# Optimization experiments

Hardware: AMD Instinct MI355X
Metric: run time of the kernel (lower is better)

## Reference

```python
import jax, jax.numpy as jnp
from jax import lax
import numpy as np

B = 8192
HID = 128
FILT = 256  # stft filter length
HOP = 128
PAD = 64
NBINS = 129  # FILT//2 + 1


def setup_inputs() -> dict:
    key = jax.random.key(0)
    ks = jax.random.split(key, 16)
    def rn(k, shape, fan_in):
        return jax.random.normal(k, shape, dtype=jnp.float32) / np.sqrt(fan_in)
    inp = {
        "audio_input": jax.random.normal(ks[0], (B, 4160), dtype=jnp.float32),
        "hidden_state": jnp.zeros((B, HID), dtype=jnp.float32),
        "cell_state": jnp.zeros((B, HID), dtype=jnp.float32),
        # STFT forward basis: [2*NBINS, 1, FILT] (real then imag banks)
        "stft_w": rn(ks[1], (2 * NBINS, 1, FILT), FILT),
        # encoder: 4 conv1d layers (out, in, k), strides 1,2,2,1, pad 1
        "enc_w1": rn(ks[2], (128, 129, 3), 129 * 3), "enc_b1": jnp.zeros((128,), jnp.float32),
        "enc_w2": rn(ks[3], (64, 128, 3), 128 * 3), "enc_b2": jnp.zeros((64,), jnp.float32),
        "enc_w3": rn(ks[4], (64, 64, 3), 64 * 3),   "enc_b3": jnp.zeros((64,), jnp.float32),
        "enc_w4": rn(ks[5], (128, 64, 3), 64 * 3),  "enc_b4": jnp.zeros((128,), jnp.float32),
        # LSTMCell (PyTorch layout): gates order i,f,g,o
        "w_ih": rn(ks[6], (4 * HID, HID), HID), "w_hh": rn(ks[7], (4 * HID, HID), HID),
        "b_ih": jnp.zeros((4 * HID,), jnp.float32), "b_hh": jnp.zeros((4 * HID,), jnp.float32),
        # output head: Linear(128 -> 1) + sigmoid
        "out_w": rn(ks[8], (1, HID), HID), "out_b": jnp.zeros((1,), jnp.float32),
    }
    return inp


def _conv1d(x, w, b, stride, pad):
    # x: [N, C_in, L], w: [C_out, C_in, k]
    y = lax.conv_general_dilated(x, w, (stride,), [(pad, pad)],
                                 dimension_numbers=("NCH", "OIH", "NCH"))
    return y + b[None, :, None]


def reference(audio_input, hidden_state, cell_state, stft_w,
              enc_w1, enc_b1, enc_w2, enc_b2, enc_w3, enc_b3, enc_w4, enc_b4,
              w_ih, w_hh, b_ih, b_hh, out_w, out_b):
    b = audio_input.shape[0]
    # chunk i with context == audio_input[:, i*512 : i*512 + 576]
    chunks = jnp.stack([audio_input[:, i * 512:i * 512 + 576] for i in range(8)], axis=0)  # [8,B,576]
    x = chunks.reshape(8 * b, 576)
    # STFT: reflect pad 64 each side, conv stride 128 -> [8B, 258, 4]
    xp = jnp.pad(x, ((0, 0), (PAD, PAD)), mode="reflect")[:, None, :]
    spec = lax.conv_general_dilated(xp, stft_w, (HOP,), "VALID",
                                    dimension_numbers=("NCH", "OIH", "NCH"))
    mag = jnp.sqrt(spec[:, :NBINS] ** 2 + spec[:, NBINS:] ** 2)  # [8B,129,4]
    # encoder conv stack: 4 -> 4 -> 2 -> 1 -> 1 frames
    h1 = jax.nn.relu(_conv1d(mag, enc_w1, enc_b1, 1, 1))
    h2 = jax.nn.relu(_conv1d(h1, enc_w2, enc_b2, 2, 1))
    h3 = jax.nn.relu(_conv1d(h2, enc_w3, enc_b3, 2, 1))
    h4 = jax.nn.relu(_conv1d(h3, enc_w4, enc_b4, 1, 1))  # [8B,128,1]
    feats = h4[:, :, 0].reshape(8, b, HID)  # [8,B,128]

    def step(carry, x_t):
        h, c = carry
        gates = x_t @ w_ih.T + b_ih + h @ w_hh.T + b_hh  # [B,4H]
        i_g, f_g, g_g, o_g = jnp.split(gates, 4, axis=-1)
        c_new = jax.nn.sigmoid(f_g) * c + jax.nn.sigmoid(i_g) * jnp.tanh(g_g)
        h_new = jax.nn.sigmoid(o_g) * jnp.tanh(c_new)
        p = jax.nn.sigmoid(h_new @ out_w.T + out_b)  # [B,1]
        return (h_new, c_new), p

    (h_fin, c_fin), probs = lax.scan(step, (hidden_state, cell_state), feats)  # probs [8,B,1]
    # final = 1 - prod_i (1 - p_i), shape [B,1,1]
    final = (1.0 - jnp.prod(1.0 - probs, axis=0))[:, :, None]
    return final, h_fin, c_fin
```

## Files before the change

### kernel.cpp

```cpp
#include <hip/hip_runtime.h>
#include <hip/hip_bf16.h>
#include <math.h>

typedef __hip_bfloat16 bf16;
typedef __attribute__((ext_vector_type(4))) float f32x4;
typedef __attribute__((ext_vector_type(8))) short short8;
typedef __attribute__((ext_vector_type(4))) short short4v;

#define BATCH   8192
#define NTOT    65536
#define NW      262144
#define HID     128

__device__ __forceinline__ float b2f(bf16 v){ return __bfloat162float(v); }
__device__ __forceinline__ bf16  f2b(float v){ return __float2bfloat16(v); }
__device__ __forceinline__ short f2bs(float v){
  bf16 b = __float2bfloat16(v);
  return *reinterpret_cast<short*>(&b);
}
__device__ __forceinline__ float sigf(float x){ return 1.0f/(1.0f+__expf(-x)); }
__device__ __forceinline__ float tanhfast(float x){
  return 1.0f - 2.0f/(__expf(2.0f*x)+1.0f);
}

__global__ __launch_bounds__(256) void k_wcvt(
    const float* __restrict__ W, bf16* __restrict__ Wb)
{
  const int idx = blockIdx.x*256 + threadIdx.x;
  if (idx < 258*256) Wb[idx] = f2b(W[idx]);
}
__global__ __launch_bounds__(256) void k_w1cvt(
    const float* __restrict__ w1, bf16* __restrict__ w1b)
{
  const int idx = blockIdx.x*256 + threadIdx.x;
  if (idx >= 61440) return;
  const int dt = idx / 20480, rem = idx % 20480;
  const int cout = rem / 160, k = rem % 160;
  const float v = (k < 129) ? w1[(cout*129 + k)*3 + dt] : 0.f;
  w1b[idx] = f2b(v);
}
__global__ __launch_bounds__(256) void k_w2cvt(
    const float* __restrict__ w2, bf16* __restrict__ w2b)
{
  const int idx = blockIdx.x*256 + threadIdx.x;
  if (idx >= 24576) return;
  const int dt = idx >> 13, cout = (idx >> 7) & 63, k = idx & 127;
  w2b[idx] = f2b(w2[(cout*128 + k)*3 + dt]);
}
__global__ __launch_bounds__(256) void k_w34cvt(
    const float* __restrict__ w3, const float* __restrict__ w4,
    bf16* __restrict__ w3e, bf16* __restrict__ w4e)
{
  const int idx = blockIdx.x*256 + threadIdx.x;
  if (idx >= 16384) return;
  if (idx < 8192){
    const int row = idx >> 7, k = idx & 127;
    const int cin = k >> 1, t = k & 1;
    w3e[idx] = f2b(w3[(row*64 + cin)*3 + 1 + t]);
  } else {
    const int i2 = idx - 8192;
    const int row = i2 >> 6, cin = i2 & 63;
    w4e[i2] = f2b(w4[(row*64 + cin)*3 + 1]);
  }
}
__global__ __launch_bounds__(256) void k_wlcvt1(
    const float* __restrict__ whh, bf16* __restrict__ wl1)
{
  const int idx = blockIdx.x*256 + threadIdx.x;
  if (idx >= 65536) return;
  wl1[idx] = f2b(whh[idx]);
}
__global__ __launch_bounds__(256) void k_wlxcvt(
    const float* __restrict__ wih, bf16* __restrict__ wlx)
{
  const int idx = blockIdx.x*256 + threadIdx.x;
  if (idx >= 65536) return;
  wlx[idx] = f2b(wih[idx]);
}

__global__ __launch_bounds__(256) void k_stft3(
    const float* __restrict__ audio, const bf16* __restrict__ Wb,
    bf16* __restrict__ mag)
{
  __shared__ __align__(16) char ALDS[96*512];
  __shared__ __align__(16) bf16 refl[4*8*64];
  const int tid = threadIdx.x, lane = tid & 63, wq = tid >> 6;
  const int r0 = blockIdx.x * 4;
  const float* arow = audio + (size_t)(r0 + wq) * 4160;

  #pragma unroll
  for (int q = 0; q < 8; ++q){
    const int e = q*64 + lane;
    const int i = e >> 6, k = e & 63;
    refl[(wq*8 + i)*64 + k] = f2b(arow[512*i + 64 - k]);
  }

  const int kgo8 = (lane>>4)*8;
  short8 Bfrag[2][8];
  #pragma unroll
  for (int ng = 0; ng < 2; ++ng){
    const int wl = ng*16 + (lane & 15);
    const int i = wl >> 2, t = wl & 3;
    #pragma unroll
    for (int ks = 0; ks < 8; ++ks){
      const int kb = ks*32 + kgo8;
      if (t == 0 && kb < 64){
        Bfrag[ng][ks] = *(const short8*)(refl + (wq*8 + i)*64 + kb);
      } else {
        const float* src = arow + 512*i + 128*t - 64 + kb;
        const float4 v0 = *(const float4*)(src);
        const float4 v1 = *(const float4*)(src + 4);
        short8 s;
        s[0]=f2bs(v0.x); s[1]=f2bs(v0.y); s[2]=f2bs(v0.z); s[3]=f2bs(v0.w);
        s[4]=f2bs(v1.x); s[5]=f2bs(v1.y); s[6]=f2bs(v1.z); s[7]=f2bs(v1.w);
        Bfrag[ng][ks] = s;
      }
    }
  }

  const int kab = (lane>>4)*16;
  for (int pass = 0; pass < 3; ++pass){
    __syncthreads();
    for (int idx = tid; idx < 96*32; idx += 256){
      const int ar = idx >> 5;
      const int cb = (idx & 31) * 16;
      const int b3 = ar >> 5, reim = (ar >> 4) & 1, bl = ar & 15;
      int bin = pass*48 + b3*16 + bl;
      if (bin > 128) bin = 128;
      const int grow = bin + reim*129;
      int off = ar*512 + cb; off ^= ((ar&7)<<4);
      *(f32x4*)(ALDS + off) = *(const f32x4*)((const char*)Wb + grow*512 + cb);
    }
    __syncthreads();

    f32x4 accRe[3][2], accIm[3][2];
    #pragma unroll
    for (int b3 = 0; b3 < 3; ++b3)
      #pragma unroll
      for (int ng = 0; ng < 2; ++ng){
        accRe[b3][ng] = f32x4{0.f,0.f,0.f,0.f};
        accIm[b3][ng] = f32x4{0.f,0.f,0.f,0.f};
      }
    #pragma unroll
    for (int ks = 0; ks < 8; ++ks){
      #pragma unroll
      for (int b3 = 0; b3 < 3; ++b3){
        const int arRe = b3*32 + (lane & 15);
        const int arIm = arRe + 16;
        int offRe = arRe*512 + ks*64 + kab; offRe ^= ((arRe&7)<<4);
        int offIm = arIm*512 + ks*64 + kab; offIm ^= ((arIm&7)<<4);
        const short8 aRe = *(const short8*)(ALDS + offRe);
        const short8 aIm = *(const short8*)(ALDS + offIm);
        #pragma unroll
        for (int ng = 0; ng < 2; ++ng){
          accRe[b3][ng] = __builtin_amdgcn_mfma_f32_16x16x32_bf16(
              aRe, Bfrag[ng][ks], accRe[b3][ng], 0, 0, 0);
          accIm[b3][ng] = __builtin_amdgcn_mfma_f32_16x16x32_bf16(
              aIm, Bfrag[ng][ks], accIm[b3][ng], 0, 0, 0);
        }
      }
    }
    #pragma unroll
    for (int b3 = 0; b3 < 3; ++b3)
      #pragma unroll
      for (int j = 0; j < 4; ++j){
        const int bin = (pass*3 + b3)*16 + (lane>>4)*4 + j;
        if (bin <= 128){
          #pragma unroll
          for (int ng = 0; ng < 2; ++ng){
            const int wl = ng*16 + (lane & 15);
            const int i = wl >> 2, t = wl & 3;
            const float re = accRe[b3][ng][j], im = accIm[b3][ng][j];
            mag[(size_t)bin*NW + (size_t)i*32768 + (r0+wq)*4 + t] =
                f2b(sqrtf(re*re + im*im));
          }
        }
      }
  }
}

#define E1_LDS (192*320)
__global__ __launch_bounds__(256) void k_enc1234(
    const bf16* __restrict__ mag,
    const bf16* __restrict__ w1b, const float* __restrict__ b1,
    const bf16* __restrict__ w2b, const float* __restrict__ b2,
    const bf16* __restrict__ w3e, const float* __restrict__ b3,
    const bf16* __restrict__ w4e, const float* __restrict__ b4,
    bf16* __restrict__ h4)
{
  __shared__ __align__(16) char Bs[E1_LDS];
  char* const B3 = Bs + 40960;
  char* const B4 = Bs + 49152;
  const int tid = threadIdx.x, lane = tid & 63, wq = tid >> 6;
  const int n0 = blockIdx.x * 32;
  const int i  = n0 >> 13, b0 = n0 & 8191;
  const size_t colbase = (size_t)i*32768 + (size_t)b0*4;
  const int kb = (lane>>4)*16;
  const int wr = wq >> 1, wc = wq & 1;

  for (int off = tid*16; off < E1_LDS; off += 256*16)
    *(f32x4*)(Bs + off) = f32x4{0.f,0.f,0.f,0.f};
  __syncthreads();
  for (int it = tid; it < 129*64; it += 256){
    const int cin = it >> 6, seg = it & 63;
    const unsigned int pair =
        *(const unsigned int*)(mag + (size_t)cin*NW + colbase + seg*2);
    #pragma unroll
    for (int q = 0; q < 2; ++q){
      const int w = seg*2 + q;
      const int row = (w>>2)*6 + (w&3) + 1;
      int off = row*320 + cin*2; off ^= ((row&7)<<4);
      *(short*)(Bs + off) = (short)((q==0) ? (pair & 0xffff) : (pair >> 16));
    }
  }
  __syncthreads();

  f32x4 acc1[4][4];
  #pragma unroll
  for (int mg = 0; mg < 4; ++mg)
    #pragma unroll
    for (int ng = 0; ng < 4; ++ng) acc1[mg][ng] = f32x4{0.f,0.f,0.f,0.f};
  int brow[4], acol[4];
  #pragma unroll
  for (int ng = 0; ng < 4; ++ng){
    const int w = wc*64 + ng*16 + (lane & 15);
    brow[ng] = (w>>2)*6 + (w&3);
  }
  #pragma unroll
  for (int mg = 0; mg < 4; ++mg) acol[mg] = wr*64 + mg*16 + (lane & 15);

  for (int dt = 0; dt < 3; ++dt){
    #pragma unroll
    for (int ks = 0; ks < 5; ++ks){
      short8 afr[4], bfr[4];
      #pragma unroll
      for (int mg = 0; mg < 4; ++mg)
        afr[mg] = *(const short8*)((const char*)w1b +
            ((dt*128 + acol[mg])*160 + ks*32)*2 + kb);
      #pragma unroll
      for (int ng = 0; ng < 4; ++ng){
        const int row = brow[ng] + dt;
        int off = row*320 + ks*64 + kb; off ^= ((row&7)<<4);
        bfr[ng] = *(const short8*)(Bs + off);
      }
      #pragma unroll
      for (int mg = 0; mg < 4; ++mg)
        #pragma unroll
        for (int ng = 0; ng < 4; ++ng)
          acc1[mg][ng] = __builtin_amdgcn_mfma_f32_16x16x32_bf16(
              afr[mg], bfr[ng], acc1[mg][ng], 0, 0, 0);
    }
  }
  __syncthreads();

  for (int it = tid; it < 32*16; it += 256){
    const int nloc = it >> 4, cb = (it & 15)*16;
    *(f32x4*)(Bs + (nloc*5)*256 + cb) = f32x4{0.f,0.f,0.f,0.f};
  }
  #pragma unroll
  for (int mg = 0; mg < 4; ++mg)
    #pragma unroll
    for (int j = 0; j < 4; ++j){
      const int cout = wr*64 + mg*16 + (lane>>4)*4 + j;
      const float bv = b1[cout];
      #pragma unroll
      for (int ng = 0; ng < 4; ++ng){
        const int w = wc*64 + ng*16 + (lane & 15);
        float v = acc1[mg][ng][j] + bv; v = v > 0.f ? v : 0.f;
        const int row5 = (w>>2)*5 + (w&3) + 1;
        int off = row5*256 + cout*2; off ^= ((row5&7)<<4);
        *(short*)(Bs + off) = f2bs(v);
      }
    }
  __syncthreads();

  f32x4 acc2[2][2];
  #pragma unroll
  for (int mg = 0; mg < 2; ++mg)
    #pragma unroll
    for (int ng = 0; ng < 2; ++ng) acc2[mg][ng] = f32x4{0.f,0.f,0.f,0.f};
  int brow2[2], acol2[2];
  #pragma unroll
  for (int ng = 0; ng < 2; ++ng){
    const int wl = wc*32 + ng*16 + (lane & 15);
    brow2[ng] = (wl>>1)*5 + (wl&1)*2;
  }
  #pragma unroll
  for (int mg = 0; mg < 2; ++mg) acol2[mg] = wr*32 + mg*16 + (lane & 15);

  for (int dt = 0; dt < 3; ++dt){
    #pragma unroll
    for (int ks = 0; ks < 4; ++ks){
      short8 afr[2], bfr[2];
      #pragma unroll
      for (int mg = 0; mg < 2; ++mg)
        afr[mg] = *(const short8*)((const char*)w2b +
            ((dt*64 + acol2[mg])*128 + ks*32)*2 + kb);
      #pragma unroll
      for (int ng = 0; ng < 2; ++ng){
        const int row = brow2[ng] + dt;
        int off = row*256 + ks*64 + kb; off ^= ((row&7)<<4);
        bfr[ng] = *(const short8*)(Bs + off);
      }
      #pragma unroll
      for (int mg = 0; mg < 2; ++mg)
        #pragma unroll
        for (int ng = 0; ng < 2; ++ng)
          acc2[mg][ng] = __builtin_amdgcn_mfma_f32_16x16x32_bf16(
              afr[mg], bfr[ng], acc2[mg][ng], 0, 0, 0);
    }
  }

  #pragma unroll
  for (int mg = 0; mg < 2; ++mg)
    #pragma unroll
    for (int j = 0; j < 4; ++j){
      const int cout2 = wr*32 + mg*16 + (lane>>4)*4 + j;
      const float bv = b2[cout2];
      #pragma unroll
      for (int ng = 0; ng < 2; ++ng){
        const int wl = wc*32 + ng*16 + (lane & 15);
        float v = acc2[mg][ng][j] + bv; v = v > 0.f ? v : 0.f;
        const int nloc = wl >> 1, tp = wl & 1;
        int off = nloc*256 + (cout2*2 + tp)*2; off ^= ((nloc&7)<<4);
        *(short*)(B3 + off) = f2bs(v);
      }
    }
  __syncthreads();

  f32x4 acc3[2];
  acc3[0] = f32x4{0.f,0.f,0.f,0.f};
  acc3[1] = f32x4{0.f,0.f,0.f,0.f};
  const int ar1 = wq*16 + (lane & 15);
  #pragma unroll
  for (int ks = 0; ks < 4; ++ks){
    const short8 a = *(const short8*)((const char*)w3e + (ar1*128 + ks*32)*2 + kb);
    #pragma unroll
    for (int ng = 0; ng < 2; ++ng){
      const int row = ng*16 + (lane & 15);
      int off = row*256 + ks*64 + kb; off ^= ((row&7)<<4);
      const short8 bfr = *(const short8*)(B3 + off);
      acc3[ng] = __builtin_amdgcn_mfma_f32_16x16x32_bf16(a, bfr, acc3[ng], 0, 0, 0);
    }
  }

  #pragma unroll
  for (int j = 0; j < 4; ++j){
    const int r1 = wq*16 + (lane>>4)*4 + j;
    const float bv = b3[r1];
    #pragma unroll
    for (int ng = 0; ng < 2; ++ng){
      const int col = ng*16 + (lane & 15);
      float v = acc3[ng][j] + bv; v = v > 0.f ? v : 0.f;
      int off = col*128 + r1*2; off ^= ((col&7)<<4);
      *(short*)(B4 + off) = f2bs(v);
    }
  }
  __syncthreads();

  f32x4 acc4[2][2];
  #pragma unroll
  for (int mg = 0; mg < 2; ++mg)
    #pragma unroll
    for (int ng = 0; ng < 2; ++ng) acc4[mg][ng] = f32x4{0.f,0.f,0.f,0.f};
  #pragma unroll
  for (int ks = 0; ks < 2; ++ks){
    short8 bfr[2];
    #pragma unroll
    for (int ng = 0; ng < 2; ++ng){
      const int row = ng*16 + (lane & 15);
      int off = row*128 + ks*64 + kb; off ^= ((row&7)<<4);
      bfr[ng] = *(const short8*)(B4 + off);
    }
    #pragma unroll
    for (int mg = 0; mg < 2; ++mg){
      const int ar2 = wq*32 + mg*16 + (lane & 15);
      const short8 a = *(const short8*)((const char*)w4e + (ar2*64 + ks*32)*2 + kb);
      #pragma unroll
      for (int ng = 0; ng < 2; ++ng)
        acc4[mg][ng] = __builtin_amdgcn_mfma_f32_16x16x32_bf16(a, bfr[ng], acc4[mg][ng], 0, 0, 0);
    }
  }
  #pragma unroll
  for (int mg = 0; mg < 2; ++mg)
    #pragma unroll
    for (int j = 0; j < 4; ++j){
      const int cout = wq*32 + mg*16 + (lane>>4)*4 + j;
      const float bv = b4[cout];
      #pragma unroll
      for (int ng = 0; ng < 2; ++ng){
        const int n = n0 + ng*16 + (lane & 15);
        float v = acc4[mg][ng][j] + bv; v = v > 0.f ? v : 0.f;
        h4[(size_t)cout*NTOT + n] = f2b(v);
      }
    }
}

__global__ __launch_bounds__(256) void k_init(
    const float* __restrict__ h0, const float* __restrict__ c0,
    float* __restrict__ hT0, float* __restrict__ cT)
{
  const int idx = blockIdx.x*256 + threadIdx.x;
  const int b = idx >> 7, c = idx & 127;
  hT0[c*BATCH + b] = h0[idx];
  cT [c*BATCH + b] = c0[idx];
}

__global__ __launch_bounds__(256) void k_gatex(
    const bf16* __restrict__ h4, const bf16* __restrict__ wlx,
    float* __restrict__ xg, int half)
{
  __shared__ __align__(16) char Bs[32*256];
  const int tid = threadIdx.x, lane = tid & 63, wq = tid >> 6;
  const int n0 = blockIdx.x * 32;
  const int gcol = half*32768 + n0;

  for (int it = tid; it < 128*32; it += 256){
    const int cp = it >> 5, nl = it & 31;
    const bf16 v = h4[(size_t)cp*NTOT + gcol + nl];
    int off = nl*256 + cp*2; off ^= ((nl&7)<<4);
    *(short*)(Bs + off) = *(const short*)&v;
  }
  __syncthreads();

  f32x4 acc[8][2];
  #pragma unroll
  for (int mg = 0; mg < 8; ++mg)
    #pragma unroll
    for (int ng = 0; ng < 2; ++ng) acc[mg][ng] = f32x4{0.f,0.f,0.f,0.f};

  int arow[8];
  #pragma unroll
  for (int mg = 0; mg < 8; ++mg) arow[mg] = wq*128 + mg*16 + (lane & 15);
  const int kb = (lane>>4)*16;

  #pragma unroll
  for (int ks = 0; ks < 4; ++ks){
    short8 bfr[2];
    #pragma unroll
    for (int ng = 0; ng < 2; ++ng){
      const int row = ng*16 + (lane & 15);
      int off = row*256 + ks*64 + kb; off ^= ((row&7)<<4);
      bfr[ng] = *(const short8*)(Bs + off);
    }
    #pragma unroll
    for (int mg = 0; mg < 8; ++mg){
      const short8 a = *(const short8*)((const char*)wlx +
          ((size_t)arow[mg]*128 + ks*32)*2 + kb);
      #pragma unroll
      for (int ng = 0; ng < 2; ++ng)
        acc[mg][ng] = __builtin_amdgcn_mfma_f32_16x16x32_bf16(
            a, bfr[ng], acc[mg][ng], 0, 0, 0);
    }
  }

  #pragma unroll
  for (int mg = 0; mg < 8; ++mg)
    #pragma unroll
    for (int j = 0; j < 4; ++j){
      const int row = wq*128 + mg*16 + (lane>>4)*4 + j;
      #pragma unroll
      for (int ng = 0; ng < 2; ++ng){
        const int col = n0 + ng*16 + (lane & 15);
        xg[(size_t)row*32768 + col] = acc[mg][ng][j];
      }
    }
}

__global__ __launch_bounds__(256) void k_lstm_rec(
    const float* __restrict__ xg, const bf16* __restrict__ wl1,
    const float* __restrict__ bih, const float* __restrict__ bhh,
    const float* __restrict__ hprev, float* __restrict__ hout,
    float* __restrict__ cT, int s)
{
  __shared__ __align__(16) char Bs[32*256];
  const int tid = threadIdx.x, lane = tid & 63, wq = tid >> 6;
  const int b0 = blockIdx.x * 32;

  for (int it = tid; it < 128*32; it += 256){
    const int cp = it >> 5, bl = it & 31;
    const float v = hprev[cp*BATCH + b0 + bl];
    int off = bl*256 + cp*2; off ^= ((bl&7)<<4);
    *(short*)(Bs + off) = f2bs(v);
  }
  __syncthreads();

  const int c0r = wq*32;
  f32x4 acc[4][2][2];
  #pragma unroll
  for (int g = 0; g < 4; ++g)
    #pragma unroll
    for (int h = 0; h < 2; ++h)
      #pragma unroll
      for (int ng = 0; ng < 2; ++ng) acc[g][h][ng] = f32x4{0.f,0.f,0.f,0.f};

  int arow[4][2];
  #pragma unroll
  for (int g = 0; g < 4; ++g)
    #pragma unroll
    for (int h = 0; h < 2; ++h)
      arow[g][h] = (g*128 + c0r + h*16 + (lane&15))*256 + (lane>>4)*16;

  #pragma unroll
  for (int ks = 0; ks < 4; ++ks){
    short8 bfr[2];
    #pragma unroll
    for (int ng = 0; ng < 2; ++ng){
      const int row = ng*16 + (lane & 15);
      int off = row*256 + ks*64 + (lane>>4)*16; off ^= ((row&7)<<4);
      bfr[ng] = *(const short8*)(Bs + off);
    }
    #pragma unroll
    for (int g = 0; g < 4; ++g)
      #pragma unroll
      for (int h = 0; h < 2; ++h){
        const short8 a = *(const short8*)((const char*)wl1 + arow[g][h] + ks*64);
        #pragma unroll
        for (int ng = 0; ng < 2; ++ng)
          acc[g][h][ng] = __builtin_amdgcn_mfma_f32_16x16x32_bf16(
              a, bfr[ng], acc[g][h][ng], 0, 0, 0);
      }
  }

  const size_t xcolbase = (size_t)(s & 3)*8192 + b0;
  #pragma unroll
  for (int h = 0; h < 2; ++h)
    #pragma unroll
    for (int ng = 0; ng < 2; ++ng)
      #pragma unroll
      for (int j = 0; j < 4; ++j){
        const int c = c0r + h*16 + (lane>>4)*4 + j;
        const int b = b0 + ng*16 + (lane & 15);
        const size_t xc = xcolbase + ng*16 + (lane & 15);
        const float ig = acc[0][h][ng][j] + xg[(size_t)(0*128+c)*32768 + xc] + bih[c]       + bhh[c];
        const float fg = acc[1][h][ng][j] + xg[(size_t)(1*128+c)*32768 + xc] + bih[128 + c] + bhh[128 + c];
        const float gg = acc[2][h][ng][j] + xg[(size_t)(2*128+c)*32768 + xc] + bih[256 + c] + bhh[256 + c];
        const float og = acc[3][h][ng][j] + xg[(size_t)(3*128+c)*32768 + xc] + bih[384 + c] + bhh[384 + c];
        const float cold = cT[c*BATCH + b];
        const float cn = sigf(fg)*cold + sigf(ig)*tanhfast(gg);
        const float hn = sigf(og)*tanhfast(cn);
        cT  [c*BATCH + b] = cn;
        hout[c*BATCH + b] = hn;
      }
}

__global__ __launch_bounds__(256) void k_headp(
    const float* __restrict__ hseq, const float* __restrict__ ow,
    const float* __restrict__ ob, float* __restrict__ P)
{
  const int idx = blockIdx.x*256 + threadIdx.x;
  const int s = idx >> 13, b = idx & (BATCH-1);
  const float* hp = hseq + (size_t)s*HID*BATCH;
  float acc = ob[0];
  for (int c = 0; c < 128; ++c) acc += ow[c]*hp[c*BATCH + b];
  P[s*BATCH + b] = sigf(acc);
}
__global__ __launch_bounds__(256) void k_head2(
    const float* __restrict__ P, float* __restrict__ outp)
{
  const int b = blockIdx.x*256 + threadIdx.x;
  float prod = 1.f;
  #pragma unroll
  for (int s = 0; s < 8; ++s) prod *= (1.f - P[s*BATCH + b]);
  outp[b] = 1.f - prod;
}

__global__ __launch_bounds__(256) void k_outT(
    const float* __restrict__ h7, const float* __restrict__ cT,
    float* __restrict__ out)
{
  const int idx = blockIdx.x*256 + threadIdx.x;
  const int b = idx >> 7, c = idx & 127;
  out[8192 + idx]           = h7[c*BATCH + b];
  out[8192 + 1048576 + idx] = cT[c*BATCH + b];
}

extern "C" void kernel_launch(void* const* d_in, const int* in_sizes, int n_in,
                              void* d_out, int out_size, void* d_ws, size_t ws_size,
                              hipStream_t stream)
{
  (void)in_sizes; (void)n_in; (void)out_size; (void)ws_size;
  const float* audio = (const float*)d_in[0];
  const float* h0    = (const float*)d_in[1];
  const float* c0    = (const float*)d_in[2];
  const float* stftw = (const float*)d_in[3];
  const float* w1 = (const float*)d_in[4];  const float* b1 = (const float*)d_in[5];
  const float* w2 = (const float*)d_in[6];  const float* b2 = (const float*)d_in[7];
  const float* w3 = (const float*)d_in[8];  const float* b3 = (const float*)d_in[9];
  const float* w4 = (const float*)d_in[10]; const float* b4 = (const float*)d_in[11];
  const float* wih = (const float*)d_in[12]; const float* whh = (const float*)d_in[13];
  const float* bih = (const float*)d_in[14]; const float* bhh = (const float*)d_in[15];
  const float* ow  = (const float*)d_in[16]; const float* ob  = (const float*)d_in[17];
  float* out = (float*)d_out;

  char* ws = (char*)d_ws;
  bf16*  Wbf  = (bf16*) (ws + 67633152);
  bf16*  h4   = (bf16*) (ws + 67633152);
  bf16*  mag  = (bf16*) (ws + 0);
  float* xg   = (float*)(ws + 0);
  float* hseq = (float*)(ws + 92274688);
  float* hT0  = (float*)(ws + 125829120);
  float* cT   = (float*)(ws + 130023424);
  bf16*  w1b  = (bf16*) (ws + 134742016);
  bf16*  w2b  = (bf16*) (ws + 134864896);
  bf16*  w3e  = (bf16*) (ws + 134914048);
  bf16*  w4e  = (bf16*) (ws + 134930432);
  bf16*  wl1  = (bf16*) (ws + 134946816);
  bf16*  wlx  = (bf16*) (ws + 135077888);
  float* Pbuf = (float*)(ws + 135397376);

  k_wcvt  <<<258, 256, 0, stream>>>(stftw, Wbf);
  k_w1cvt <<<240, 256, 0, stream>>>(w1, w1b);
  k_w2cvt <<<96, 256, 0, stream>>>(w2, w2b);
  k_w34cvt<<<64, 256, 0, stream>>>(w3, w4, w3e, w4e);
  k_wlcvt1<<<256, 256, 0, stream>>>(whh, wl1);
  k_wlxcvt<<<256, 256, 0, stream>>>(wih, wlx);
  k_init  <<<4096, 256, 0, stream>>>(h0, c0, hT0, cT);
  k_stft3<<<2048, 256, 0, stream>>>(audio, Wbf, mag);
  k_enc1234<<<2048, 256, 0, stream>>>(mag, w1b, b1, w2b, b2, w3e, b3,
                                      w4e, b4, h4);
  for (int half = 0; half < 2; ++half){
    k_gatex<<<1024, 256, 0, stream>>>(h4, wlx, xg, half);
    for (int q = 0; q < 4; ++q){
      const int s = half*4 + q;
      const float* hprev = (s == 0) ? hT0 : (hseq + (size_t)(s-1)*HID*BATCH);
      k_lstm_rec<<<256, 256, 0, stream>>>(xg, wl1, bih, bhh, hprev,
                                          hseq + (size_t)s*HID*BATCH, cT, s);
    }
  }
  k_headp<<<256, 256, 0, stream>>>(hseq, ow, ob, Pbuf);
  k_head2<<<32, 256, 0, stream>>>(Pbuf, out);
  k_outT<<<4096, 256, 0, stream>>>(hseq + (size_t)7*HID*BATCH, cT, out);
}
```

Measured before the change: 435.4 us.

## Fuse all LSTM timesteps, head and output transpose into one persistent kernel

Replaces the eight per-step recurrent launches, the init transpose, the head kernels and the output transpose with one kernel. Each block keeps its 32-sample slice of h in LDS and c in registers across all eight steps, and accumulates the output-head probability product on chip. The input-gate buffer is enlarged to hold all eight steps so both gatex launches run before the recurrence. This removes repeated global round trips of h and c and about a dozen launches. In exchange, only 256 blocks do the whole sequential recurrence, a larger workspace is needed, and the final h and c are written with strided stores.

Result: no change. 430.0 us (-1.2%).

```diff
diff --git a/kernel.cpp b/kernel.cpp
--- a/kernel.cpp
+++ b/kernel.cpp
@@ -396,16 +396,6 @@
     }
 }
 
-__global__ __launch_bounds__(256) void k_init(
-    const float* __restrict__ h0, const float* __restrict__ c0,
-    float* __restrict__ hT0, float* __restrict__ cT)
-{
-  const int idx = blockIdx.x*256 + threadIdx.x;
-  const int b = idx >> 7, c = idx & 127;
-  hT0[c*BATCH + b] = h0[idx];
-  cT [c*BATCH + b] = c0[idx];
-}
-
 __global__ __launch_bounds__(256) void k_gatex(
     const bf16* __restrict__ h4, const bf16* __restrict__ wlx,
     float* __restrict__ xg, int half)
@@ -461,38 +451,48 @@
       const int row = wq*128 + mg*16 + (lane>>4)*4 + j;
       #pragma unroll
       for (int ng = 0; ng < 2; ++ng){
-        const int col = n0 + ng*16 + (lane & 15);
-        xg[(size_t)row*32768 + col] = acc[mg][ng][j];
-      }
-    }
-}
-
-__global__ __launch_bounds__(256) void k_lstm_rec(
+        const int col = gcol + ng*16 + (lane & 15);
+        xg[(size_t)row*65536 + col] = acc[mg][ng][j];
+      }
+    }
+}
+
+__global__ __launch_bounds__(256) void k_lstm_all2(
     const float* __restrict__ xg, const bf16* __restrict__ wl1,
     const float* __restrict__ bih, const float* __restrict__ bhh,
-    const float* __restrict__ hprev, float* __restrict__ hout,
-    float* __restrict__ cT, int s)
+    const float* __restrict__ h0, const float* __restrict__ c0,
+    const float* __restrict__ ow, const float* __restrict__ ob,
+    float* __restrict__ out)
 {
   __shared__ __align__(16) char Bs[32*256];
+  __shared__ float Ppart[16*32];
+  __shared__ float Pprod[32];
   const int tid = threadIdx.x, lane = tid & 63, wq = tid >> 6;
   const int b0 = blockIdx.x * 32;
+  const int c0r = wq*32;
 
   for (int it = tid; it < 128*32; it += 256){
     const int cp = it >> 5, bl = it & 31;
-    const float v = hprev[cp*BATCH + b0 + bl];
+    const float v = h0[(size_t)(b0 + bl)*128 + cp];
     int off = bl*256 + cp*2; off ^= ((bl&7)<<4);
     *(short*)(Bs + off) = f2bs(v);
   }
-  __syncthreads();
-
-  const int c0r = wq*32;
-  f32x4 acc[4][2][2];
-  #pragma unroll
-  for (int g = 0; g < 4; ++g)
-    #pragma unroll
-    for (int h = 0; h < 2; ++h)
-      #pragma unroll
-      for (int ng = 0; ng < 2; ++ng) acc[g][h][ng] = f32x4{0.f,0.f,0.f,0.f};
+  float cst[2][2][4], bsum[4][2][4], owv[2][4];
+  #pragma unroll
+  for (int h = 0; h < 2; ++h)
+    #pragma unroll
+    for (int j = 0; j < 4; ++j){
+      const int c = c0r + h*16 + (lane>>4)*4 + j;
+      owv[h][j] = ow[c];
+      #pragma unroll
+      for (int g = 0; g < 4; ++g)
+        bsum[g][h][j] = bih[g*128 + c] + bhh[g*128 + c];
+      #pragma unroll
+      for (int ng = 0; ng < 2; ++ng)
+        cst[h][ng][j] = c0[(size_t)(b0 + ng*16 + (lane & 15))*128 + c];
+    }
+  if (tid < 32) Pprod[tid] = 1.f;
+  const float obv = ob[0];
 
   int arow[4][2];
   #pragma unroll
@@ -501,78 +501,76 @@
     for (int h = 0; h < 2; ++h)
       arow[g][h] = (g*128 + c0r + h*16 + (lane&15))*256 + (lane>>4)*16;
 
-  #pragma unroll
-  for (int ks = 0; ks < 4; ++ks){
-    short8 bfr[2];
-    #pragma unroll
-    for (int ng = 0; ng < 2; ++ng){
-      const int row = ng*16 + (lane & 15);
-      int off = row*256 + ks*64 + (lane>>4)*16; off ^= ((row&7)<<4);
-      bfr[ng] = *(const short8*)(Bs + off);
-    }
+  __syncthreads();
+
+  for (int s = 0; s < 8; ++s){
+    f32x4 acc[4][2][2];
     #pragma unroll
     for (int g = 0; g < 4; ++g)
       #pragma unroll
-      for (int h = 0; h < 2; ++h){
-        const short8 a = *(const short8*)((const char*)wl1 + arow[g][h] + ks*64);
+      for (int h = 0; h < 2; ++h)
         #pragma unroll
-        for (int ng = 0; ng < 2; ++ng)
-          acc[g][h][ng] = __builtin_amdgcn_mfma_f32_16x16x32_bf16(
-              a, bfr[ng], acc[g][h][ng], 0, 0, 0);
-      }
-  }
-
-  const size_t xcolbase = (size_t)(s & 3)*8192 + b0;
-  #pragma unroll
-  for (int h = 0; h < 2; ++h)
-    #pragma unroll
-    for (int ng = 0; ng < 2; ++ng)
-      #pragma unroll
-      for (int j = 0; j < 4; ++j){
-        const int c = c0r + h*16 + (lane>>4)*4 + j;
-        const int b = b0 + ng*16 + (lane & 15);
-        const size_t xc = xcolbase + ng*16 + (lane & 15);
-        const float ig = acc[0][h][ng][j] + xg[(size_t)(0*128+c)*32768 + xc] + bih[c]       + bhh[c];
-        const float fg = acc[1][h][ng][j] + xg[(size_t)(1*128+c)*32768 + xc] + bih[128 + c] + bhh[128 + c];
-        const float gg = acc[2][h][ng][j] + xg[(size_t)(2*128+c)*32768 + xc] + bih[256 + c] + bhh[256 + c];
-        const float og = acc[3][h][ng][j] + xg[(size_t)(3*128+c)*32768 + xc] + bih[384 + c] + bhh[384 + c];
-        const float cold = cT[c*BATCH + b];
-        const float cn = sigf(fg)*cold + sigf(ig)*tanhfast(gg);
-        const float hn = sigf(og)*tanhfast(cn);
-        cT  [c*BATCH + b] = cn;
-        hout[c*BATCH + b] = hn;
-      }
-}
-
-__global__ __launch_bounds__(256) void k_headp(
-    const float* __restrict__ hseq, const float* __restrict__ ow,
-    const float* __restrict__ ob, float* __restrict__ P)
-{
-  const int idx = blockIdx.x*256 + threadIdx.x;
-  const int s = idx >> 13, b = idx & (BATCH-1);
-  const float* hp = hseq + (size_t)s*HID*BATCH;
-  float acc = ob[0];
-  for (int c = 0; c < 128; ++c) acc += ow[c]*hp[c*BATCH + b];
-  P[s*BATCH + b] = sigf(acc);
-}
-__global__ __launch_bounds__(256) void k_head2(
-    const float* __restrict__ P, float* __restrict__ outp)
-{
-  const int b = blockIdx.x*256 + threadIdx.x;
-  float prod = 1.f;
-  #pragma unroll
-  for (int s = 0; s < 8; ++s) prod *= (1.f - P[s*BATCH + b]);
-  outp[b] = 1.f - prod;
-}
-
-__global__ __launch_bounds__(256) void k_outT(
-    const float* __restrict__ h7, const float* __restrict__ cT,
-    float* __restrict__ out)
-{
-  const int idx = blockIdx.x*256 + threadIdx.x;
-  const int b = idx >> 7, c = idx & 127;
-  out[8192 + idx]           = h7[c*BATCH + b];
-  out[8192 + 1048576 + idx] = cT[c*BATCH + b];
+        for (int ng = 0; ng < 2; ++ng) acc[g][h][ng] = f32x4{0.f,0.f,0.f,0.f};
+    #pragma unroll
+    for (int ks = 0; ks < 4; ++ks){
+      short8 bfr[2];
+      #pragma unroll
+      for (int ng = 0; ng < 2; ++ng){
+        const int row = ng*16 + (lane & 15);
+        int off = row*256 + ks*64 + (lane>>4)*16; off ^= ((row&7)<<4);
+        bfr[ng] = *(const short8*)(Bs + off);
+      }
+      #pragma unroll
+      for (int g = 0; g < 4; ++g)
+        #pragma unroll
+        for (int h = 0; h < 2; ++h){
+          const short8 a = *(const short8*)((const char*)wl1 + arow[g][h] + ks*64);
+          #pragma unroll
+          for (int ng = 0; ng < 2; ++ng)
+            acc[g][h][ng] = __builtin_amdgcn_mfma_f32_16x16x32_bf16(
+                a, bfr[ng], acc[g][h][ng], 0, 0, 0);
+        }
+    }
+    __syncthreads();
+
+    float psum0 = 0.f, psum1 = 0.f;
+    #pragma unroll
+    for (int h = 0; h < 2; ++h)
+      #pragma unroll
+      for (int ng = 0; ng < 2; ++ng)
+        #pragma unroll
+        for (int j = 0; j < 4; ++j){
+          const int c = c0r + h*16 + (lane>>4)*4 + j;
+          const int b = b0 + ng*16 + (lane & 15);
+          const size_t xc = (size_t)s*8192 + b;
+          const float ig = acc[0][h][ng][j] + xg[(size_t)(0*128+c)*65536 + xc] + bsum[0][h][j];
+          const float fg = acc[1][h][ng][j] + xg[(size_t)(1*128+c)*65536 + xc] + bsum[1][h][j];
+          const float gg = acc[2][h][ng][j] + xg[(size_t)(2*128+c)*65536 + xc] + bsum[2][h][j];
+          const float og = acc[3][h][ng][j] + xg[(size_t)(3*128+c)*65536 + xc] + bsum[3][h][j];
+          const float cn = sigf(fg)*cst[h][ng][j] + sigf(ig)*tanhfast(gg);
+          const float hn = sigf(og)*tanhfast(cn);
+          cst[h][ng][j] = cn;
+          const float pw = owv[h][j] * hn;
+          if (ng == 0) psum0 += pw; else psum1 += pw;
+          const int bl = ng*16 + (lane & 15);
+          int off = bl*256 + c*2; off ^= ((bl&7)<<4);
+          *(short*)(Bs + off) = f2bs(hn);
+          if (s == 7){
+            out[8192 + (size_t)b*128 + c]           = hn;
+            out[8192 + 1048576 + (size_t)b*128 + c] = cn;
+          }
+        }
+    Ppart[(wq*4 + (lane>>4))*32 + (lane & 15)]      = psum0;
+    Ppart[(wq*4 + (lane>>4))*32 + 16 + (lane & 15)] = psum1;
+    __syncthreads();
+    if (tid < 32){
+      float a2 = obv;
+      #pragma unroll
+      for (int q2 = 0; q2 < 16; ++q2) a2 += Ppart[q2*32 + tid];
+      Pprod[tid] *= (1.f - sigf(a2));
+    }
+  }
+  if (tid < 32) out[b0 + tid] = 1.f - Pprod[tid];
 }
 
 extern "C" void kernel_launch(void* const* d_in, const int* in_sizes, int n_in,
@@ -594,20 +592,16 @@
   float* out = (float*)d_out;
 
   char* ws = (char*)d_ws;
-  bf16*  Wbf  = (bf16*) (ws + 67633152);
-  bf16*  h4   = (bf16*) (ws + 67633152);
+  float* xg   = (float*)(ws + 0);
   bf16*  mag  = (bf16*) (ws + 0);
-  float* xg   = (float*)(ws + 0);
-  float* hseq = (float*)(ws + 92274688);
-  float* hT0  = (float*)(ws + 125829120);
-  float* cT   = (float*)(ws + 130023424);
-  bf16*  w1b  = (bf16*) (ws + 134742016);
-  bf16*  w2b  = (bf16*) (ws + 134864896);
-  bf16*  w3e  = (bf16*) (ws + 134914048);
-  bf16*  w4e  = (bf16*) (ws + 134930432);
-  bf16*  wl1  = (bf16*) (ws + 134946816);
-  bf16*  wlx  = (bf16*) (ws + 135077888);
-  float* Pbuf = (float*)(ws + 135397376);
+  bf16*  h4   = (bf16*) (ws + 134217728);
+  bf16*  Wbf  = (bf16*) (ws + 134217728);
+  bf16*  w1b  = (bf16*) (ws + 150994944);
+  bf16*  w2b  = (bf16*) (ws + 151117824);
+  bf16*  w3e  = (bf16*) (ws + 151166976);
+  bf16*  w4e  = (bf16*) (ws + 151183360);
+  bf16*  wl1  = (bf16*) (ws + 151199744);
+  bf16*  wlx  = (bf16*) (ws + 151330816);
 
   k_wcvt  <<<258, 256, 0, stream>>>(stftw, Wbf);
   k_w1cvt <<<240, 256, 0, stream>>>(w1, w1b);
@@ -615,20 +609,10 @@
   k_w34cvt<<<64, 256, 0, stream>>>(w3, w4, w3e, w4e);
   k_wlcvt1<<<256, 256, 0, stream>>>(whh, wl1);
   k_wlxcvt<<<256, 256, 0, stream>>>(wih, wlx);
-  k_init  <<<4096, 256, 0, stream>>>(h0, c0, hT0, cT);
   k_stft3<<<2048, 256, 0, stream>>>(audio, Wbf, mag);
   k_enc1234<<<2048, 256, 0, stream>>>(mag, w1b, b1, w2b, b2, w3e, b3,
                                       w4e, b4, h4);
-  for (int half = 0; half < 2; ++half){
-    k_gatex<<<1024, 256, 0, stream>>>(h4, wlx, xg, half);
-    for (int q = 0; q < 4; ++q){
-      const int s = half*4 + q;
-      const float* hprev = (s == 0) ? hT0 : (hseq + (size_t)(s-1)*HID*BATCH);
-      k_lstm_rec<<<256, 256, 0, stream>>>(xg, wl1, bih, bhh, hprev,
-                                          hseq + (size_t)s*HID*BATCH, cT, s);
-    }
-  }
-  k_headp<<<256, 256, 0, stream>>>(hseq, ow, ob, Pbuf);
-  k_head2<<<32, 256, 0, stream>>>(Pbuf, out);
-  k_outT<<<4096, 256, 0, stream>>>(hseq + (size_t)7*HID*BATCH, cT, out);
-}
+  k_gatex<<<1024, 256, 0, stream>>>(h4, wlx, xg, 0);
+  k_gatex<<<1024, 256, 0, stream>>>(h4, wlx, xg, 1);
+  k_lstm_all2<<<256, 256, 0, stream>>>(xg, wl1, bih, bhh, h0, c0, ow, ob, out);
+}
```
